# Kernel tuning notes

Measured on AMD Instinct MI355X. Metric: run time of the kernel, lower is better.

The kernel has to match this reference:

```python
import jax, jax.numpy as jnp
import numpy as np

N = 8192
IN_DIM = 256
OUT_DIM = 256
NEG_INF = -1000000000.0
LEAKY_SLOPE = 0.2


def setup_inputs() -> dict:
    key = jax.random.key(0)
    k_h, k_adj, k_W, k_a = jax.random.split(key, 4)
    h = jax.random.normal(k_h, (N, IN_DIM), dtype=jnp.float32)
    adj = jax.random.randint(k_adj, (N, N), 0, 2, dtype=jnp.int32)
    # learned params (nn.Linear without bias stores weight [out, in]; we keep [in, out] for x @ W)
    W = jax.random.normal(k_W, (IN_DIM, OUT_DIM), dtype=jnp.float32) / np.sqrt(IN_DIM)
    a = jax.random.normal(k_a, (OUT_DIM,), dtype=jnp.float32) / np.sqrt(OUT_DIM)
    return {"h": h, "adj": adj, "W": W, "a": a}


def reference(h, adj, W, a):
    Wh = h @ W                                   # [N, out_dim]
    f = Wh @ a                                   # [N]
    e = jax.nn.leaky_relu(f[:, None] + f[None, :], LEAKY_SLOPE)  # [N, N]
    mask = (adj > 0).astype(Wh.dtype)
    e_masked = e * mask + (1.0 - mask) * NEG_INF
    alpha = jax.nn.softmax(e_masked, axis=1)     # [N, N]
    h_prime = alpha @ Wh                         # [N, out_dim]
    return jax.nn.elu(h_prime), alpha
```

## Files before the change

kernel.cpp:

```cpp
#include <hip/hip_runtime.h>
#include <hip/hip_bf16.h>

#define NROW 8192
#define DIM 256

typedef short bf16x8 __attribute__((ext_vector_type(8)));
typedef float f32x4 __attribute__((ext_vector_type(4)));

__device__ __forceinline__ short f2bf(float x) {
    return __builtin_bit_cast(short, __float2bfloat16(x));
}

__device__ __forceinline__ void gload_lds16(const void* g, void* l) {
    __builtin_amdgcn_global_load_lds(
        (const __attribute__((address_space(1))) unsigned int*)g,
        (__attribute__((address_space(3))) unsigned int*)l, 16, 0, 0);
}

__global__ __launch_bounds__(256) void k1_whgemm(
    const float* __restrict__ h, const float* __restrict__ W,
    const float* __restrict__ a, short* __restrict__ whbT,
    float* __restrict__ f)
{
    __shared__ float hs[64][65];
    __shared__ float wsm[64][65];
    const int tid = threadIdx.x;
    const int tx = tid & 15, ty = tid >> 4;
    const int i0 = blockIdx.x * 64;
    const int n0 = blockIdx.y * 64;

    float acc[4][4];
#pragma unroll
    for (int u = 0; u < 4; ++u)
#pragma unroll
        for (int v = 0; v < 4; ++v) acc[u][v] = 0.f;

    for (int kb = 0; kb < DIM; kb += 64) {
#pragma unroll
        for (int rr = 0; rr < 4; ++rr) {
            int row = rr * 16 + ty;
            *(float4*)&hs[row][tx * 4] =
                *(const float4*)&h[(size_t)(i0 + row) * DIM + kb + tx * 4];
            *(float4*)&wsm[row][tx * 4] =
                *(const float4*)&W[(size_t)(kb + row) * DIM + n0 + tx * 4];
        }
        __syncthreads();
#pragma unroll 8
        for (int kk = 0; kk < 64; ++kk) {
            float av[4], bv[4];
#pragma unroll
            for (int u = 0; u < 4; ++u) av[u] = hs[ty * 4 + u][kk];
#pragma unroll
            for (int v = 0; v < 4; ++v) bv[v] = wsm[kk][tx * 4 + v];
#pragma unroll
            for (int u = 0; u < 4; ++u)
#pragma unroll
                for (int v = 0; v < 4; ++v) acc[u][v] += av[u] * bv[v];
        }
        __syncthreads();
    }

#pragma unroll
    for (int u = 0; u < 4; ++u)
#pragma unroll
        for (int v = 0; v < 4; ++v) hs[ty * 4 + u][tx * 4 + v] = acc[u][v];
    __syncthreads();

    {
        int r = tid >> 2, q = tid & 3;
        float s = 0.f;
#pragma unroll
        for (int c = 0; c < 16; ++c) s += hs[r][q * 16 + c] * a[n0 + q * 16 + c];
        s += __shfl_xor(s, 1);
        s += __shfl_xor(s, 2);
        if (q == 0) atomicAdd(&f[i0 + r], s);
    }

    {
        int n = tid >> 2, q = tid & 3;
        union { short s[16]; int4 i4[2]; } pk;
#pragma unroll
        for (int b = 0; b < 4; ++b)
#pragma unroll
            for (int c = 0; c < 4; ++c)
                pk.s[b * 4 + c] = f2bf(hs[q * 16 + b * 4 + c][n]);
        size_t base = ((size_t)(i0 >> 6) * 256 + n0 + n) * 64 + q * 16;
        *(int4*)&whbT[base] = pk.i4[0];
        *(int4*)&whbT[base + 8] = pk.i4[1];
    }
}

__global__ __launch_bounds__(256) void k3d_alpha(
    const int* __restrict__ adj, const float* __restrict__ f,
    float* __restrict__ alpha)
{
    const int i = blockIdx.x;
    const int tid = threadIdx.x;
    const float fi = f[i];
    const int* row = adj + (size_t)i * NROW;

    int4 av[8];
    float4 fv[8];
#pragma unroll
    for (int it = 0; it < 8; ++it)
        av[it] = *(const int4*)&row[it * 1024 + tid * 4];
#pragma unroll
    for (int it = 0; it < 8; ++it)
        fv[it] = *(const float4*)&f[it * 1024 + tid * 4];

    float sum = 0.f;
#pragma unroll
    for (int it = 0; it < 8; ++it) {
        float x0 = fi + fv[it].x, x1 = fi + fv[it].y;
        float x2 = fi + fv[it].z, x3 = fi + fv[it].w;
        float4 t;
        t.x = av[it].x > 0 ? __expf(fmaxf(x0, 0.2f * x0)) : 0.f;
        t.y = av[it].y > 0 ? __expf(fmaxf(x1, 0.2f * x1)) : 0.f;
        t.z = av[it].z > 0 ? __expf(fmaxf(x2, 0.2f * x2)) : 0.f;
        t.w = av[it].w > 0 ? __expf(fmaxf(x3, 0.2f * x3)) : 0.f;
        fv[it] = t;
        sum += t.x + t.y + t.z + t.w;
    }

#pragma unroll
    for (int off = 32; off > 0; off >>= 1) sum += __shfl_xor(sum, off);
    __shared__ float red[4];
    if ((tid & 63) == 0) red[tid >> 6] = sum;
    __syncthreads();
    const float inv = 1.f / (red[0] + red[1] + red[2] + red[3]);

    float* arow = alpha + (size_t)i * NROW;
#pragma unroll
    for (int it = 0; it < 8; ++it) {
        float4 t = fv[it];
        float4 o = {t.x * inv, t.y * inv, t.z * inv, t.w * inv};
        *(float4*)&arow[it * 1024 + tid * 4] = o;
    }
}

__global__ __launch_bounds__(512, 2) void k4e_gemm(
    const float* __restrict__ alpha, const short* __restrict__ whbT,
    float* __restrict__ out0)
{
    __shared__ __align__(16) short Bs[4][16384];

    const int tid = threadIdx.x;
    const int wave = tid >> 6;
    const int lane = tid & 63;
    const int lo = lane & 15;
    const int quad = lane >> 4;
    const int q8 = quad * 8;
    const int rg = wave & 1;
    const int cg = wave >> 1;
    const int i0 = blockIdx.x * 32;

    const float* aptr = alpha + (size_t)(i0 + rg * 16 + lo) * NROW + q8;

    const int srow = lane >> 3;
    const int swz = ((lane & 7) ^ srow) * 8;

    const int bx0 = (quad ^ (lo & 7)) * 8;
    const int bx1 = ((4 + quad) ^ (lo & 7)) * 8;
    int off0[4], off1[4];
#pragma unroll
    for (int nt = 0; nt < 4; ++nt) {
        int rb = (cg * 64 + nt * 16 + lo) * 64;
        off0[nt] = rb + bx0;
        off1[nt] = rb + bx1;
    }

    f32x4 acc[4] = {};
    f32x4 aA[4], aB[4], aC[4], aD[4];

#define STAGE(buf, kt)                                                        \
    {                                                                         \
        const short* gtile = whbT + (size_t)(kt) * 16384;                     \
        _Pragma("unroll")                                                     \
        for (int s = 0; s < 4; ++s)                                           \
            gload_lds16(gtile + ((wave * 4 + s) * 8 + srow) * 64 + swz,       \
                        &Bs[buf][(wave * 4 + s) * 512]);                      \
    }

#define ALOAD(set, kt)                                                        \
    {                                                                         \
        const float* ap = aptr + (size_t)(kt) * 64;                           \
        asm volatile("global_load_dwordx4 %0, %4, off\n\t"                    \
                     "global_load_dwordx4 %1, %4, off offset:16\n\t"          \
                     "global_load_dwordx4 %2, %4, off offset:128\n\t"         \
                     "global_load_dwordx4 %3, %4, off offset:144"             \
                     : "=&v"(aA[set]), "=&v"(aB[set]),                        \
                       "=&v"(aC[set]), "=&v"(aD[set])                         \
                     : "v"(ap));                                              \
    }

#define CONSUME(c)                                                            \
    {                                                                         \
        bf16x8 af0, af1;                                                      \
        af0[0] = f2bf(aA[c][0]); af0[1] = f2bf(aA[c][1]);                     \
        af0[2] = f2bf(aA[c][2]); af0[3] = f2bf(aA[c][3]);                     \
        af0[4] = f2bf(aB[c][0]); af0[5] = f2bf(aB[c][1]);                     \
        af0[6] = f2bf(aB[c][2]); af0[7] = f2bf(aB[c][3]);                     \
        af1[0] = f2bf(aC[c][0]); af1[1] = f2bf(aC[c][1]);                     \
        af1[2] = f2bf(aC[c][2]); af1[3] = f2bf(aC[c][3]);                     \
        af1[4] = f2bf(aD[c][0]); af1[5] = f2bf(aD[c][1]);                     \
        af1[6] = f2bf(aD[c][2]); af1[7] = f2bf(aD[c][3]);                     \
        _Pragma("unroll")                                                     \
        for (int nt = 0; nt < 4; ++nt) {                                      \
            bf16x8 b0 = *(const bf16x8*)&Bs[c][off0[nt]];                     \
            acc[nt] = __builtin_amdgcn_mfma_f32_16x16x32_bf16(af0, b0,        \
                                                          acc[nt], 0, 0, 0);  \
            bf16x8 b1 = *(const bf16x8*)&Bs[c][off1[nt]];                     \
            acc[nt] = __builtin_amdgcn_mfma_f32_16x16x32_bf16(af1, b1,        \
                                                          acc[nt], 0, 0, 0);  \
        }                                                                     \
    }

#define KSTEP_FULL(kt, c)                                                     \
    {                                                                         \
        STAGE(((c) + 2) & 3, (kt) + 2);                                       \
        ALOAD(((c) + 2) & 3, (kt) + 2);                                       \
        asm volatile("s_waitcnt vmcnt(16)" ::: "memory");                     \
        __builtin_amdgcn_s_barrier();                                         \
        __builtin_amdgcn_sched_barrier(0);                                    \
        CONSUME(c)                                                            \
    }

    STAGE(0, 0); ALOAD(0, 0);
    STAGE(1, 1); ALOAD(1, 1);

#pragma unroll 1
    for (int base = 0; base < 124; base += 4) {
        KSTEP_FULL(base + 0, 0)
        KSTEP_FULL(base + 1, 1)
        KSTEP_FULL(base + 2, 2)
        KSTEP_FULL(base + 3, 3)
    }
    KSTEP_FULL(124, 0)
    KSTEP_FULL(125, 1)
    asm volatile("s_waitcnt vmcnt(8)" ::: "memory");
    __builtin_amdgcn_s_barrier();
    __builtin_amdgcn_sched_barrier(0);
    CONSUME(2)
    asm volatile("s_waitcnt vmcnt(0)" ::: "memory");
    __builtin_amdgcn_s_barrier();
    __builtin_amdgcn_sched_barrier(0);
    CONSUME(3)

#undef STAGE
#undef ALOAD
#undef CONSUME
#undef KSTEP_FULL

    const int ccb = cg * 64 + lo;
#pragma unroll
    for (int nt = 0; nt < 4; ++nt) {
#pragma unroll
        for (int c = 0; c < 4; ++c) {
            const int rr = i0 + rg * 16 + quad * 4 + c;
            float v = acc[nt][c];
            v = v > 0.f ? v : __expf(v) - 1.f;
            out0[(size_t)rr * DIM + ccb + nt * 16] = v;
        }
    }
}

extern "C" void kernel_launch(void* const* d_in, const int* in_sizes, int n_in,
                              void* d_out, int out_size, void* d_ws, size_t ws_size,
                              hipStream_t stream) {
    const float* h = (const float*)d_in[0];
    const int* adj = (const int*)d_in[1];
    const float* W = (const float*)d_in[2];
    const float* a = (const float*)d_in[3];
    float* out0 = (float*)d_out;
    float* alpha = out0 + (size_t)NROW * DIM;

    char* ws = (char*)d_ws;
    float* f = (float*)ws;
    short* whbT = (short*)(ws + 32768);

    hipMemsetAsync(f, 0, NROW * sizeof(float), stream);
    k1_whgemm<<<dim3(NROW / 64, DIM / 64), 256, 0, stream>>>(h, W, a, whbT, f);
    k3d_alpha<<<dim3(NROW), 256, 0, stream>>>(adj, f, alpha);
    k4e_gemm<<<dim3(NROW / 32), 512, 0, stream>>>(alpha, whbT, out0);
}
```

Before: 638.8 us.

## Retile alpha@Wh GEMM to 128x64 tiles with XCD-aware block mapping

Changes the final GEMM so each block computes 128 rows by 64 output columns instead of 32 rows by all 256 columns. Block indices are remapped so blocks sharing the same alpha rows land on the same XCD, aiming for L2 reuse of alpha. The LDS B tile shrinks and occupancy hints change. The risk is that alpha rows are now fetched by four blocks, which may increase memory traffic if L2 reuse fails.

After: 607.7 us. 1.05x faster.

```diff
diff --git a/kernel.cpp b/kernel.cpp
--- a/kernel.cpp
+++ b/kernel.cpp
@@ -138,11 +138,11 @@
     }
 }
 
-__global__ __launch_bounds__(512, 2) void k4e_gemm(
+__global__ __launch_bounds__(512) void k4g_gemm(
     const float* __restrict__ alpha, const short* __restrict__ whbT,
     float* __restrict__ out0)
 {
-    __shared__ __align__(16) short Bs[4][16384];
+    __shared__ __align__(16) short Bs[4][4096];
 
     const int tid = threadIdx.x;
     const int wave = tid >> 6;
@@ -150,23 +150,28 @@
     const int lo = lane & 15;
     const int quad = lane >> 4;
     const int q8 = quad * 8;
-    const int rg = wave & 1;
-    const int cg = wave >> 1;
-    const int i0 = blockIdx.x * 32;
-
-    const float* aptr = alpha + (size_t)(i0 + rg * 16 + lo) * NROW + q8;
-
-    const int srow = lane >> 3;
-    const int swz = ((lane & 7) ^ srow) * 8;
+
+    const int bid = blockIdx.x;
+    const int xcd = bid & 7;
+    const int slot = bid >> 3;
+    const int rb = xcd * 8 + (slot & 7);
+    const int cs = slot >> 3;
+    const int i0 = rb * 128;
+    const int n0 = cs * 64;
+
+    const float* aptr = alpha + (size_t)(i0 + wave * 16 + lo) * NROW + q8;
+
+    const int n_local = tid >> 3;
+    const int schunk = ((tid & 7) ^ (n_local & 7)) * 8;
 
     const int bx0 = (quad ^ (lo & 7)) * 8;
     const int bx1 = ((4 + quad) ^ (lo & 7)) * 8;
     int off0[4], off1[4];
 #pragma unroll
     for (int nt = 0; nt < 4; ++nt) {
-        int rb = (cg * 64 + nt * 16 + lo) * 64;
-        off0[nt] = rb + bx0;
-        off1[nt] = rb + bx1;
+        int rbase = (nt * 16 + lo) * 64;
+        off0[nt] = rbase + bx0;
+        off1[nt] = rbase + bx1;
     }
 
     f32x4 acc[4] = {};
@@ -174,11 +179,9 @@
 
 #define STAGE(buf, kt)                                                        \
     {                                                                         \
-        const short* gtile = whbT + (size_t)(kt) * 16384;                     \
-        _Pragma("unroll")                                                     \
-        for (int s = 0; s < 4; ++s)                                           \
-            gload_lds16(gtile + ((wave * 4 + s) * 8 + srow) * 64 + swz,       \
-                        &Bs[buf][(wave * 4 + s) * 512]);                      \
+        const short* gsrc = whbT + (size_t)(kt) * 16384 +                     \
+                            (n0 + n_local) * 64 + schunk;                     \
+        gload_lds16(gsrc, &Bs[buf][tid * 8]);                                 \
     }
 
 #define ALOAD(set, kt)                                                        \
@@ -215,11 +218,11 @@
         }                                                                     \
     }
 
-#define KSTEP_FULL(kt, c)                                                     \
-    {                                                                         \
-        STAGE(((c) + 2) & 3, (kt) + 2);                                       \
-        ALOAD(((c) + 2) & 3, (kt) + 2);                                       \
-        asm volatile("s_waitcnt vmcnt(16)" ::: "memory");                     \
+#define KSTEP(kt, c, DO, N)                                                   \
+    {                                                                         \
+        if (DO) { STAGE(((c) + 2) & 3, (kt) + 2); ALOAD(((c) + 2) & 3,        \
+                                                        (kt) + 2); }          \
+        asm volatile("s_waitcnt vmcnt(" #N ")" ::: "memory");                 \
         __builtin_amdgcn_s_barrier();                                         \
         __builtin_amdgcn_sched_barrier(0);                                    \
         CONSUME(c)                                                            \
@@ -230,33 +233,27 @@
 
 #pragma unroll 1
     for (int base = 0; base < 124; base += 4) {
-        KSTEP_FULL(base + 0, 0)
-        KSTEP_FULL(base + 1, 1)
-        KSTEP_FULL(base + 2, 2)
-        KSTEP_FULL(base + 3, 3)
-    }
-    KSTEP_FULL(124, 0)
-    KSTEP_FULL(125, 1)
-    asm volatile("s_waitcnt vmcnt(8)" ::: "memory");
-    __builtin_amdgcn_s_barrier();
-    __builtin_amdgcn_sched_barrier(0);
-    CONSUME(2)
-    asm volatile("s_waitcnt vmcnt(0)" ::: "memory");
-    __builtin_amdgcn_s_barrier();
-    __builtin_amdgcn_sched_barrier(0);
-    CONSUME(3)
+        KSTEP(base + 0, 0, true, 10)
+        KSTEP(base + 1, 1, true, 10)
+        KSTEP(base + 2, 2, true, 10)
+        KSTEP(base + 3, 3, true, 10)
+    }
+    KSTEP(124, 0, true, 10)
+    KSTEP(125, 1, true, 10)
+    KSTEP(126, 2, false, 5)
+    KSTEP(127, 3, false, 0)
 
 #undef STAGE
 #undef ALOAD
 #undef CONSUME
-#undef KSTEP_FULL
-
-    const int ccb = cg * 64 + lo;
+#undef KSTEP
+
+    const int ccb = n0 + lo;
 #pragma unroll
     for (int nt = 0; nt < 4; ++nt) {
 #pragma unroll
         for (int c = 0; c < 4; ++c) {
-            const int rr = i0 + rg * 16 + quad * 4 + c;
+            const int rr = i0 + wave * 16 + quad * 4 + c;
             float v = acc[nt][c];
             v = v > 0.f ? v : __expf(v) - 1.f;
             out0[(size_t)rr * DIM + ccb + nt * 16] = v;
@@ -281,5 +278,5 @@
     hipMemsetAsync(f, 0, NROW * sizeof(float), stream);
     k1_whgemm<<<dim3(NROW / 64, DIM / 64), 256, 0, stream>>>(h, W, a, whbT, f);
     k3d_alpha<<<dim3(NROW), 256, 0, stream>>>(adj, f, alpha);
-    k4e_gemm<<<dim3(NROW / 32), 512, 0, stream>>>(alpha, whbT, out0);
-}
+    k4g_gemm<<<dim3(256), 512, 0, stream>>>(alpha, whbT, out0);
+}
```
